# Optimization experiments

Hardware: AMD Instinct MI355X
Metric: run time of the kernel (lower is better)

## Reference

```python
import jax, jax.numpy as jnp
import numpy as np

B, N, M, DIN, HID, L, NC, NH = 8, 1024, 8, 1024, 256, 2, 7, 4
DH = HID // NH
ALPHA = 0.1          # LeakyReLU slope in RGATLayer
NEG = -9e15          # masked-softmax fill value from the source


def setup_inputs() -> dict:
    key = jax.random.key(0)
    ks = jax.random.split(key, 40)
    f32 = jnp.float32
    rn = lambda k, s, sc: jax.random.normal(k, s, f32) * sc
    w = HID ** -0.5
    inp = {
        'x': rn(ks[0], (B, N, DIN), 1.0),
        'adj': jax.random.randint(ks[1], (B, N, N), 0, 2, jnp.int32),
        's_mask': jax.random.randint(ks[2], (B, N, N), 0, 2, jnp.int32),
        's_feature': rn(ks[3], (B, M, DIN), 1.0),
        's_adj': jax.random.uniform(ks[4], (B, M, N), f32),
        'speaker_id': jax.random.randint(ks[5], (B, N), 0, M, jnp.int32),
        'fc1_w': rn(ks[6], (DIN, HID), DIN ** -0.5), 'fc1_b': jnp.zeros((HID,), f32),
        'fc2_w': rn(ks[7], (DIN, HID), DIN ** -0.5), 'fc2_b': jnp.zeros((HID,), f32),
        'gat_W': rn(ks[8], (L, HID, HID), w),
        'gat_a': rn(ks[9], (L, 3 * HID), (3 * HID) ** -0.5),
        'rel_emb': rn(ks[10], (L, 2, HID), 0.1),
        'gru_wz': rn(ks[11], (L, HID, HID), 0.1), 'gru_uz': rn(ks[12], (L, HID, HID), 0.1),
        'gru_wr': rn(ks[13], (L, HID, HID), 0.1), 'gru_ur': rn(ks[14], (L, HID, HID), 0.1),
        'gru_w': rn(ks[15], (L, HID, HID), 0.1), 'gru_u': rn(ks[16], (L, HID, HID), 0.1),
        'mha_wv': rn(ks[17], (L, HID, HID), w), 'mha_bv': jnp.zeros((L, HID), f32),
        'mha_wk': rn(ks[18], (L, HID, HID), w), 'mha_bk': jnp.zeros((L, HID), f32),
        'mha_wq': rn(ks[19], (L, HID, HID), w), 'mha_bq': jnp.zeros((L, HID), f32),
        'mha_wo': rn(ks[20], (L, HID, HID), w), 'mha_bo': jnp.zeros((L, HID), f32),
        'ln_g': jnp.ones((L, HID), f32), 'ln_b': jnp.zeros((L, HID), f32),
        'out_w': rn(ks[21], (HID, NC), w), 'out_b': jnp.zeros((NC,), f32),
    }
    return inp


def _layer_norm(x, g, b):
    mu = jnp.mean(x, -1, keepdims=True)
    var = jnp.mean((x - mu) ** 2, -1, keepdims=True)
    return (x - mu) * jax.lax.rsqrt(var + 1e-5) * g + b


def reference(x, adj, s_mask, s_feature, s_adj, speaker_id,
              fc1_w, fc1_b, fc2_w, fc2_b,
              gat_W, gat_a, rel_emb,
              gru_wz, gru_uz, gru_wr, gru_ur, gru_w, gru_u,
              mha_wv, mha_bv, mha_wk, mha_bk, mha_wq, mha_bq, mha_wo, mha_bo,
              ln_g, ln_b, out_w, out_b):
    # eval mode: dropout is identity. init_way == 'global', att_agg == True.
    H = jax.nn.relu(x @ fc1_w + fc1_b)           # [B,N,HID]
    P = jax.nn.relu(s_feature @ fc2_w + fc2_b)   # [B,M,HID]
    adj_mask = adj > 0
    for l in range(L):
        P_l_1 = jnp.einsum('bmn,bmd->bnd', s_adj, P)  # s_adj^T @ P -> [B,N,HID]
        # ---- RGAT layer (decomposed: never materializes [B,N,N,3*HID]) ----
        h = H @ gat_W[l]                               # [B,N,HID]
        a1, a2, a3 = jnp.split(gat_a[l], 3)
        rel_sc = rel_emb[l] @ a3                       # (2,) per-relation score
        e = jax.nn.leaky_relu((h @ a1)[:, :, None] + (h @ a2)[:, None, :]
                              + jnp.take(rel_sc, s_mask), ALPHA)  # [B,N,N]
        att = jax.nn.softmax(jnp.where(adj_mask, e, jnp.float32(NEG)), axis=2)
        Agg = jax.nn.elu(att @ h)                      # [B,N,HID]
        # ---- Multi-head attention aggregation (replicates source's reshape) ----
        V = (H @ mha_wv[l] + mha_bv[l]).reshape(B * NH, -1, DH)
        Km = (P_l_1 @ mha_wk[l] + mha_bk[l]).reshape(B * NH, -1, DH)
        Qm = (Agg @ mha_wq[l] + mha_bq[l]).reshape(B * NH, -1, DH)
        att2 = jax.nn.softmax(jnp.einsum('bqd,bkd->bqk', Qm, Km) * DH ** -0.5, axis=-1)
        ctx = (att2 @ V).reshape(B, -1, HID)
        H_new = _layer_norm(ctx @ mha_wo[l] + mha_bo[l] + H, ln_g[l], ln_b[l])
        # ---- GRU3d speaker-state update (uses H[l], i.e. pre-update H) ----
        P_agg = jnp.einsum('bmn,bnd->bmd', s_adj, H)   # [B,M,HID]
        z = jax.nn.sigmoid(P @ gru_wz[l] + P_agg @ gru_uz[l])
        r = jax.nn.sigmoid(P @ gru_wr[l] + P_agg @ gru_ur[l])
        h_hat = jnp.tanh(P @ gru_w[l] + r * (P_agg @ gru_u[l]))
        P = (1 - z) * P + z * h_hat
        H = H_new
    # sim_loss
    ps = jnp.einsum('bmd,bkd->bmk', P, P)
    ps = ps * (1.0 - jnp.eye(M, dtype=ps.dtype))
    p_sim = jnp.mean(jnp.mean(jnp.mean(ps, -1), -1), -1)
    logits = H @ out_w + out_b
    return (logits, p_sim)
```

## Files before the change

### kernel.cpp

```cpp
#include <hip/hip_runtime.h>
#include <cmath>

#define B 8
#define N 1024
#define MSP 8
#define DIN 1024
#define HID 256
#define NLAYER 2
#define NCLS 7
#define NHEAD 4
#define DHD 64
#define G (B*NHEAD)
#define SEQ 1024
#define LALPHA 0.1f
#define NEGF (-9e15f)
#define RROWS 8

typedef unsigned short u16;
typedef unsigned int u32;
typedef __attribute__((ext_vector_type(8))) short short8;
typedef __attribute__((ext_vector_type(4))) float f32x4;

__device__ __forceinline__ u16 f2bf(float f) {
  u32 u = __float_as_uint(f);
  u += 0x7FFFu + ((u >> 16) & 1u);
  return (u16)(u >> 16);
}
__device__ __forceinline__ float bf2f(u16 v) {
  return __uint_as_float(((u32)v) << 16);
}
__device__ __forceinline__ void stf(float* p, size_t i, float v) { p[i] = v; }
__device__ __forceinline__ void stf(u16* p, size_t i, float v) { p[i] = f2bf(v); }

__device__ __forceinline__ float wave_reduce_sum(float v) {
  #pragma unroll
  for (int o = 32; o > 0; o >>= 1) v += __shfl_xor(v, o, 64);
  return v;
}
__device__ __forceinline__ float wave_reduce_max(float v) {
  #pragma unroll
  for (int o = 32; o > 0; o >>= 1) v = fmaxf(v, __shfl_xor(v, o, 64));
  return v;
}

__device__ __forceinline__ void tcast_tile(
    const float* src, u16* dst, int ldS, int ldD, int r0, int c0, int t,
    u16* tile )
{
  #pragma unroll
  for (int i = 0; i < 4; ++i) {
    int e = i * 1024 + t * 4;
    int r = e >> 6, c = e & 63;
    float4 v = *(const float4*)&src[(size_t)(r0 + r) * ldS + c0 + c];
    u16* d = &tile[r * 72 + c];
    d[0] = f2bf(v.x); d[1] = f2bf(v.y); d[2] = f2bf(v.z); d[3] = f2bf(v.w);
  }
  __syncthreads();
  #pragma unroll
  for (int i = 0; i < 2; ++i) {
    int e = i * 2048 + t * 8;
    int r2 = e >> 6, c2 = e & 63;
    u16 v[8];
    #pragma unroll
    for (int j = 0; j < 8; ++j) v[j] = tile[(c2 + j) * 72 + r2];
    *(uint4*)&dst[(size_t)(c0 + r2) * ldD + r0 + c2] = *(const uint4*)v;
  }
}

__global__ __launch_bounds__(256) void wprep256(
    const float* g, const float* wv, const float* wk, const float* wq,
    const float* wo, const float* wz, const float* wr, const float* w,
    const float* uz, const float* ur, const float* u, u16* WT)
{
  __shared__ u16 tile[64 * 72];
  int z = blockIdx.z, idx = z >> 1, l = z & 1;
  const float* src;
  switch (idx) {
    case 0: src = g; break;  case 1: src = wv; break; case 2: src = wk; break;
    case 3: src = wq; break; case 4: src = wo; break; case 5: src = wz; break;
    case 6: src = wr; break; case 7: src = w; break;  case 8: src = uz; break;
    case 9: src = ur; break; default: src = u; break;
  }
  src += (size_t)l * 65536;
  u16* dst = WT + (size_t)z * 65536;
  tcast_tile(src, dst, 256, 256, blockIdx.x * 64, blockIdx.y * 64, threadIdx.x, tile);
}

__global__ __launch_bounds__(256) void wprepfc(
    const float* w1, const float* w2, u16* WTfc)
{
  __shared__ u16 tile[64 * 72];
  int z = blockIdx.z;
  const float* src = z ? w2 : w1;
  u16* dst = WTfc + (size_t)z * 262144;
  tcast_tile(src, dst, 256, 1024, blockIdx.x * 64, blockIdx.y * 64, threadIdx.x, tile);
}

__global__ __launch_bounds__(256) void utransp_kernel(
    const u16* __restrict__ src, u16* __restrict__ dst, int ldS, int ldD)
{
  __shared__ u16 tile[64 * 72];
  int r0 = blockIdx.x * 64, c0 = blockIdx.y * 64;
  int t = threadIdx.x;
  #pragma unroll
  for (int i = 0; i < 2; ++i) {
    int e = i * 256 + t;
    int sr = e >> 3, d8 = (e & 7) * 8;
    *(uint4*)&tile[sr * 72 + d8] = *(const uint4*)&src[(size_t)(r0 + sr) * ldS + c0 + d8];
  }
  __syncthreads();
  #pragma unroll
  for (int i = 0; i < 2; ++i) {
    int e = i * 256 + t;
    int dr = e >> 3, s8 = (e & 7) * 8;
    u16 v[8];
    #pragma unroll
    for (int j = 0; j < 8; ++j) v[j] = tile[(s8 + j) * 72 + dr];
    *(uint4*)&dst[(size_t)(c0 + dr) * ldD + r0 + s8] = *(const uint4*)v;
  }
}

__global__ __launch_bounds__(256) void outprep(const float* ow, u16* WTout) {
  int t = threadIdx.x;
  for (int e = t; e < NCLS * 256; e += 256) {
    int n = e >> 8, k = e & 255;
    WTout[e] = f2bf(ow[k * NCLS + n]);
  }
}

__device__ __forceinline__ void stage_a(const float* p, u16* d) {
  #pragma unroll
  for (int q = 0; q < 4; ++q) {
    float4 v = *(const float4*)(p + q * 4);
    d[q * 4 + 0] = f2bf(v.x); d[q * 4 + 1] = f2bf(v.y);
    d[q * 4 + 2] = f2bf(v.z); d[q * 4 + 3] = f2bf(v.w);
  }
}
__device__ __forceinline__ void stage_a(const u16* p, u16* d) {
  *(uint4*)d = *(const uint4*)p;
  *(uint4*)(d + 8) = *(const uint4*)(p + 8);
}

template <typename TA, typename TC>
__global__ __launch_bounds__(256) void gemm_t(
    const TA* __restrict__ A, const TA* __restrict__ A2, int zsplit,
    const u16* __restrict__ Wt, const u16* __restrict__ Wt2,
    const float* __restrict__ bias, const float* __restrict__ bias2,
    TC* __restrict__ C,
    int K, int ldA, int ldW, int Nc, int act,
    size_t sA, size_t sW, size_t sC)
{
  __shared__ u16 As[64 * 72];
  __shared__ u16 Ws[64 * 72];
  int z = blockIdx.z;
  const TA* Ab; const u16* Wb; const float* bs;
  if (z < zsplit) {
    Ab = A + (size_t)z * sA; Wb = Wt + (size_t)z * sW; bs = bias;
  } else {
    int z2 = z - zsplit;
    Ab = A2 + (size_t)z2 * sA; Wb = Wt2 + (size_t)z2 * sW; bs = bias2;
  }
  TC* Cb = C + (size_t)z * sC;
  int bm = blockIdx.x * 64, bn = blockIdx.y * 64;
  int t = threadIdx.x;
  int w = t >> 6, lane = t & 63, quad = lane >> 4, l15 = lane & 15;
  int wy = w >> 1, wx = w & 1;
  int sr = t >> 2, kg = (t & 3) * 16;
  bool wok = (bn + sr) < Nc;
  f32x4 acc[2][2];
  #pragma unroll
  for (int i = 0; i < 2; ++i)
    #pragma unroll
    for (int j = 0; j < 2; ++j) acc[i][j] = (f32x4){0.f, 0.f, 0.f, 0.f};

  for (int k0 = 0; k0 < K; k0 += 64) {
    u16 av[16];
    stage_a(Ab + (size_t)(bm + sr) * ldA + k0 + kg, av);
    *(uint4*)&As[sr * 72 + kg] = *(const uint4*)av;
    *(uint4*)&As[sr * 72 + kg + 8] = *(const uint4*)(av + 8);
    if (wok) {
      *(uint4*)&Ws[sr * 72 + kg] = *(const uint4*)(Wb + (size_t)(bn + sr) * ldW + k0 + kg);
      *(uint4*)&Ws[sr * 72 + kg + 8] = *(const uint4*)(Wb + (size_t)(bn + sr) * ldW + k0 + kg + 8);
    } else {
      uint4 zz = {0, 0, 0, 0};
      *(uint4*)&Ws[sr * 72 + kg] = zz;
      *(uint4*)&Ws[sr * 72 + kg + 8] = zz;
    }
    __syncthreads();
    #pragma unroll
    for (int kh = 0; kh < 64; kh += 32) {
      short8 a0 = *(const short8*)&As[(wy * 32 + l15) * 72 + kh + quad * 8];
      short8 a1 = *(const short8*)&As[(wy * 32 + 16 + l15) * 72 + kh + quad * 8];
      short8 b0 = *(const short8*)&Ws[(wx * 32 + l15) * 72 + kh + quad * 8];
      short8 b1 = *(const short8*)&Ws[(wx * 32 + 16 + l15) * 72 + kh + quad * 8];
      acc[0][0] = __builtin_amdgcn_mfma_f32_16x16x32_bf16(a0, b0, acc[0][0], 0, 0, 0);
      acc[0][1] = __builtin_amdgcn_mfma_f32_16x16x32_bf16(a0, b1, acc[0][1], 0, 0, 0);
      acc[1][0] = __builtin_amdgcn_mfma_f32_16x16x32_bf16(a1, b0, acc[1][0], 0, 0, 0);
      acc[1][1] = __builtin_amdgcn_mfma_f32_16x16x32_bf16(a1, b1, acc[1][1], 0, 0, 0);
    }
    __syncthreads();
  }
  #pragma unroll
  for (int sa = 0; sa < 2; ++sa) {
    #pragma unroll
    for (int sb = 0; sb < 2; ++sb) {
      int col = bn + wx * 32 + sb * 16 + l15;
      if (col < Nc) {
        float bv = bs ? bs[col] : 0.f;
        #pragma unroll
        for (int r = 0; r < 4; ++r) {
          int row = bm + wy * 32 + sa * 16 + quad * 4 + r;
          float v = acc[sa][sb][r] + bv;
          if (act == 1) v = fmaxf(v, 0.f);
          else if (act == 2) v = (v > 0.f) ? v : (__expf(v) - 1.f);
          stf(Cb, (size_t)row * Nc + col, v);
        }
      }
    }
  }
}

__global__ __launch_bounds__(256) void fc2_reduce(
    const float* __restrict__ scr, const float* __restrict__ bias,
    float* __restrict__ out)
{
  int i = blockIdx.x * 256 + threadIdx.x;
  float v = scr[i] + scr[16384 + i] + scr[32768 + i] + scr[49152 + i]
          + bias[threadIdx.x];
  out[i] = fmaxf(v, 0.f);
}

__global__ __launch_bounds__(256) void gru_combine(
    const float* __restrict__ zP, const float* __restrict__ zU,
    const float* __restrict__ P, float* __restrict__ Pn)
{
  int i = blockIdx.x * 256 + threadIdx.x;
  float z = 1.f / (1.f + __expf(-(zP[i] + zU[i])));
  float r = 1.f / (1.f + __expf(-(zP[16384 + i] + zU[16384 + i])));
  float hh = tanhf(zP[32768 + i] + r * zU[32768 + i]);
  Pn[i] = (1.f - z) * P[i] + z * hh;
}

__global__ __launch_bounds__(256) void pl1_kernel(
    const float* __restrict__ s_adj, const float* __restrict__ P,
    float* __restrict__ out)
{
  int bn = blockIdx.x;
  int b = bn >> 10, n = bn & 1023, t = threadIdx.x;
  float acc = 0.f;
  #pragma unroll
  for (int m = 0; m < MSP; ++m) {
    float sa = s_adj[(size_t)(b * MSP + m) * N + n];
    acc += sa * P[(size_t)(b * MSP + m) * HID + t];
  }
  out[(size_t)bn * HID + t] = acc;
}

__global__ __launch_bounds__(256) void relsc_kernel(
    const float* __restrict__ rel_emb_l, const float* __restrict__ a3,
    float* __restrict__ rsc)
{
  __shared__ float scratch[4];
  int r = blockIdx.x, t = threadIdx.x;
  float v = rel_emb_l[r * HID + t] * a3[t];
  int wave = t >> 6, lane = t & 63;
  v = wave_reduce_sum(v);
  if (lane == 0) scratch[wave] = v;
  __syncthreads();
  if (t == 0) rsc[r] = scratch[0] + scratch[1] + scratch[2] + scratch[3];
}

__global__ __launch_bounds__(256) void f1f2_kernel(
    const u16* __restrict__ h, const float* __restrict__ a12,
    float* __restrict__ f1, float* __restrict__ f2)
{
  __shared__ float s1[4], s2[4];
  int row = blockIdx.x, t = threadIdx.x;
  float hv = bf2f(h[(size_t)row * HID + t]);
  float v1 = hv * a12[t];
  float v2 = hv * a12[HID + t];
  int wave = t >> 6, lane = t & 63;
  v1 = wave_reduce_sum(v1);
  v2 = wave_reduce_sum(v2);
  if (lane == 0) { s1[wave] = v1; s2[wave] = v2; }
  __syncthreads();
  if (t == 0) f1[row] = s1[0] + s1[1] + s1[2] + s1[3];
  if (t == 1) f2[row] = s2[0] + s2[1] + s2[2] + s2[3];
}

__global__ __launch_bounds__(256) void rgat_scores_kernel(
    const int* __restrict__ adj, const int* __restrict__ smask,
    const float* __restrict__ f1, const float* __restrict__ f2,
    const float* __restrict__ rsc, u16* __restrict__ Pw)
{
  __shared__ float red[4][RROWS];
  int blk = blockIdx.x;
  int b = blk / (N / RROWS);
  int i0 = (blk % (N / RROWS)) * RROWS;
  int t = threadIdx.x;
  int wave = t >> 6, lane = t & 63;
  float r0 = rsc[0], r1 = rsc[1];
  int j0 = t * 4;
  float4 f2v = *(const float4*)&f2[b * N + j0];
  float ev[RROWS][4];
  #pragma unroll
  for (int r = 0; r < RROWS; ++r) {
    size_t base = ((size_t)(b * N + i0 + r)) * N + j0;
    int4 a4 = *(const int4*)&adj[base];
    int4 s4 = *(const int4*)&smask[base];
    float f1v = f1[b * N + i0 + r];
    float e;
    e = f1v + f2v.x + (s4.x ? r1 : r0); e = (e > 0.f) ? e : LALPHA * e;
    ev[r][0] = (a4.x > 0) ? e : NEGF;
    e = f1v + f2v.y + (s4.y ? r1 : r0); e = (e > 0.f) ? e : LALPHA * e;
    ev[r][1] = (a4.y > 0) ? e : NEGF;
    e = f1v + f2v.z + (s4.z ? r1 : r0); e = (e > 0.f) ? e : LALPHA * e;
    ev[r][2] = (a4.z > 0) ? e : NEGF;
    e = f1v + f2v.w + (s4.w ? r1 : r0); e = (e > 0.f) ? e : LALPHA * e;
    ev[r][3] = (a4.w > 0) ? e : NEGF;
  }
  #pragma unroll
  for (int r = 0; r < RROWS; ++r) {
    float m = fmaxf(fmaxf(ev[r][0], ev[r][1]), fmaxf(ev[r][2], ev[r][3]));
    m = wave_reduce_max(m);
    if (lane == 0) red[wave][r] = m;
  }
  __syncthreads();
  float mx[RROWS];
  #pragma unroll
  for (int r = 0; r < RROWS; ++r)
    mx[r] = fmaxf(fmaxf(red[0][r], red[1][r]), fmaxf(red[2][r], red[3][r]));
  __syncthreads();
  #pragma unroll
  for (int r = 0; r < RROWS; ++r) {
    float s = 0.f;
    #pragma unroll
    for (int c = 0; c < 4; ++c) { ev[r][c] = __expf(ev[r][c] - mx[r]); s += ev[r][c]; }
    s = wave_reduce_sum(s);
    if (lane == 0) red[wave][r] = s;
  }
  __syncthreads();
  #pragma unroll
  for (int r = 0; r < RROWS; ++r) {
    float inv = 1.f / (red[0][r] + red[1][r] + red[2][r] + red[3][r]);
    u16 o[4];
    #pragma unroll
    for (int c = 0; c < 4; ++c) o[c] = f2bf(ev[r][c] * inv);
    *(uint2*)&Pw[((size_t)(b * N + i0 + r)) * N + j0] = *(const uint2*)o;
  }
}

__global__ __launch_bounds__(256) void vtransp_kernel(
    const u16* __restrict__ Vb, u16* __restrict__ Vt)
{
  __shared__ u16 tile[64 * 72];
  int g = blockIdx.x >> 4;
  int s0 = (blockIdx.x & 15) * 64;
  int t = threadIdx.x;
  #pragma unroll
  for (int i = 0; i < 2; ++i) {
    int e = i * 256 + t;
    int sr = e >> 3, d8 = (e & 7) * 8;
    *(uint4*)&tile[sr * 72 + d8] =
        *(const uint4*)&Vb[((size_t)(g * SEQ) + s0 + sr) * DHD + d8];
  }
  __syncthreads();
  #pragma unroll
  for (int i = 0; i < 2; ++i) {
    int e = i * 256 + t;
    int dr = e >> 3, s8 = (e & 7) * 8;
    u16 v[8];
    #pragma unroll
    for (int j = 0; j < 8; ++j) v[j] = tile[(s8 + j) * 72 + dr];
    *(uint4*)&Vt[((size_t)(g * DHD) + dr) * SEQ + s0 + s8] = *(const uint4*)v;
  }
}

__global__ __launch_bounds__(256) void mha_mfma_kernel(
    const u16* __restrict__ Qb, const u16* __restrict__ Kb,
    const u16* __restrict__ Vt, float* __restrict__ ctx)
{
  __shared__ u16 Ks[64 * 72];
  __shared__ u16 Vs[64 * 72];
  __shared__ u16 Ps[4][16 * 72];
  int g = blockIdx.x >> 4;
  int q0 = (blockIdx.x & 15) * 64;
  int t = threadIdx.x;
  int w = t >> 6, lane = t & 63, quad = lane >> 4, l15 = lane & 15;
  const u16* Qrow = Qb + ((size_t)(g * SEQ) + q0 + w * 16 + l15) * DHD;
  short8 qa0 = *(const short8*)(Qrow + quad * 8);
  short8 qa1 = *(const short8*)(Qrow + 32 + quad * 8);
  const u16* Kg = Kb + (size_t)g * SEQ * DHD;
  const u16* Vg = Vt + (size_t)g * DHD * SEQ;
  f32x4 O[4];
  #pragma unroll
  for (int nt = 0; nt < 4; ++nt) O[nt] = (f32x4){0.f, 0.f, 0.f, 0.f};
  float mprev[4] = {-1e30f, -1e30f, -1e30f, -1e30f};
  float lsum[4] = {0.f, 0.f, 0.f, 0.f};

  for (int kc = 0; kc < SEQ; kc += 64) {
    #pragma unroll
    for (int i = 0; i < 2; ++i) {
      int e = i * 256 + t;
      int row = e >> 3, c8 = (e & 7) * 8;
      *(uint4*)&Ks[row * 72 + c8] = *(const uint4*)&Kg[(size_t)(kc + row) * DHD + c8];
      *(uint4*)&Vs[row * 72 + c8] = *(const uint4*)&Vg[(size_t)row * SEQ + kc + c8];
    }
    __syncthreads();
    f32x4 s[4];
    #pragma unroll
    for (int st = 0; st < 4; ++st) {
      short8 b0 = *(const short8*)&Ks[(st * 16 + l15) * 72 + quad * 8];
      short8 b1 = *(const short8*)&Ks[(st * 16 + l15) * 72 + 32 + quad * 8];
      f32x4 c = (f32x4){0.f, 0.f, 0.f, 0.f};
      c = __builtin_amdgcn_mfma_f32_16x16x32_bf16(qa0, b0, c, 0, 0, 0);
      c = __builtin_amdgcn_mfma_f32_16x16x32_bf16(qa1, b1, c, 0, 0, 0);
      s[st] = c * 0.125f;
    }
    float cm[4];
    #pragma unroll
    for (int r = 0; r < 4; ++r)
      cm[r] = fmaxf(fmaxf(s[0][r], s[1][r]), fmaxf(s[2][r], s[3][r]));
    #pragma unroll
    for (int off = 1; off < 16; off <<= 1) {
      #pragma unroll
      for (int r = 0; r < 4; ++r) cm[r] = fmaxf(cm[r], __shfl_xor(cm[r], off, 64));
    }
    float mnew[4], alpha[4], rs[4];
    #pragma unroll
    for (int r = 0; r < 4; ++r) {
      mnew[r] = fmaxf(mprev[r], cm[r]);
      alpha[r] = __expf(mprev[r] - mnew[r]);
      mprev[r] = mnew[r];
      rs[r] = 0.f;
    }
    #pragma unroll
    for (int st = 0; st < 4; ++st) {
      #pragma unroll
      for (int r = 0; r < 4; ++r) {
        float p = __expf(s[st][r] - mnew[r]);
        rs[r] += p;
        Ps[w][(quad * 4 + r) * 72 + st * 16 + l15] = f2bf(p);
      }
    }
    #pragma unroll
    for (int off = 1; off < 16; off <<= 1) {
      #pragma unroll
      for (int r = 0; r < 4; ++r) rs[r] += __shfl_xor(rs[r], off, 64);
    }
    #pragma unroll
    for (int r = 0; r < 4; ++r) lsum[r] = lsum[r] * alpha[r] + rs[r];
    #pragma unroll
    for (int nt = 0; nt < 4; ++nt)
      #pragma unroll
      for (int r = 0; r < 4; ++r) O[nt][r] *= alpha[r];
    #pragma unroll
    for (int kh = 0; kh < 2; ++kh) {
      short8 pa = *(const short8*)&Ps[w][l15 * 72 + kh * 32 + quad * 8];
      #pragma unroll
      for (int nt = 0; nt < 4; ++nt) {
        short8 vb = *(const short8*)&Vs[(nt * 16 + l15) * 72 + kh * 32 + quad * 8];
        O[nt] = __builtin_amdgcn_mfma_f32_16x16x32_bf16(pa, vb, O[nt], 0, 0, 0);
      }
    }
    __syncthreads();
  }
  #pragma unroll
  for (int nt = 0; nt < 4; ++nt) {
    #pragma unroll
    for (int r = 0; r < 4; ++r) {
      size_t row = (size_t)(g * SEQ) + q0 + w * 16 + quad * 4 + r;
      ctx[row * DHD + nt * 16 + l15] = O[nt][r] / lsum[r];
    }
  }
}

__global__ __launch_bounds__(256) void ln_kernel(
    const float* __restrict__ tmp, const float* __restrict__ Hres,
    const float* __restrict__ gg, const float* __restrict__ bb,
    float* __restrict__ out)
{
  __shared__ float s1[4], s2[4];
  int row = blockIdx.x, t = threadIdx.x;
  float x = tmp[(size_t)row * HID + t] + Hres[(size_t)row * HID + t];
  float v1 = wave_reduce_sum(x);
  float v2 = wave_reduce_sum(x * x);
  int wave = t >> 6, lane = t & 63;
  if (lane == 0) { s1[wave] = v1; s2[wave] = v2; }
  __syncthreads();
  float mu = (s1[0] + s1[1] + s1[2] + s1[3]) * (1.f / HID);
  float var = (s2[0] + s2[1] + s2[2] + s2[3]) * (1.f / HID) - mu * mu;
  var = fmaxf(var, 0.f);
  float y = (x - mu) * rsqrtf(var + 1e-5f) * gg[t] + bb[t];
  out[(size_t)row * HID + t] = y;
}

__global__ __launch_bounds__(256) void pagg_part(
    const float* __restrict__ s_adj, const float* __restrict__ H,
    float* __restrict__ scr)
{
  int row = blockIdx.x;
  int sl = blockIdx.y;
  int b = row >> 3, t = threadIdx.x;
  const float* Hb = H + ((size_t)(b * N) + sl * 128) * HID + t;
  const float* sa = s_adj + (size_t)row * N + sl * 128;
  float acc = 0.f;
  #pragma unroll 4
  for (int n = 0; n < 128; ++n)
    acc += sa[n] * Hb[(size_t)n * HID];
  scr[((size_t)sl * (B * MSP) + row) * HID + t] = acc;
}
__global__ __launch_bounds__(256) void pagg_reduce(
    const float* __restrict__ scr, float* __restrict__ Pagg)
{
  int row = blockIdx.x, t = threadIdx.x;
  float s = 0.f;
  #pragma unroll
  for (int k = 0; k < 8; ++k) s += scr[((size_t)k * (B * MSP) + row) * HID + t];
  Pagg[(size_t)row * HID + t] = s;
}

__global__ __launch_bounds__(256) void psim_kernel(
    const float* __restrict__ P, float* __restrict__ out)
{
  __shared__ float scratch[4];
  int t = threadIdx.x;
  float total = 0.f;
  for (int idx = t; idx < B * MSP * MSP; idx += 256) {
    int b = idx >> 6, m = (idx >> 3) & 7, k = idx & 7;
    if (m != k) {
      const float* pm = P + (size_t)(b * MSP + m) * HID;
      const float* pk = P + (size_t)(b * MSP + k) * HID;
      float d = 0.f;
      for (int dd = 0; dd < HID; ++dd) d += pm[dd] * pk[dd];
      total += d;
    }
  }
  int wave = t >> 6, lane = t & 63;
  total = wave_reduce_sum(total);
  if (lane == 0) scratch[wave] = total;
  __syncthreads();
  if (t == 0)
    out[0] = (scratch[0] + scratch[1] + scratch[2] + scratch[3]) *
             (1.f / (B * MSP * MSP));
}

extern "C" void kernel_launch(void* const* d_in, const int* in_sizes, int n_in,
                              void* d_out, int out_size, void* d_ws, size_t ws_size,
                              hipStream_t stream) {
  const float* x      = (const float*)d_in[0];
  const int*   adj    = (const int*)d_in[1];
  const int*   smask  = (const int*)d_in[2];
  const float* s_feat = (const float*)d_in[3];
  const float* s_adj  = (const float*)d_in[4];
  const float* fc1_w  = (const float*)d_in[6];
  const float* fc1_b  = (const float*)d_in[7];
  const float* fc2_w  = (const float*)d_in[8];
  const float* fc2_b  = (const float*)d_in[9];
  const float* gat_W  = (const float*)d_in[10];
  const float* gat_a  = (const float*)d_in[11];
  const float* rel_emb= (const float*)d_in[12];
  const float* gru_wz = (const float*)d_in[13];
  const float* gru_uz = (const float*)d_in[14];
  const float* gru_wr = (const float*)d_in[15];
  const float* gru_ur = (const float*)d_in[16];
  const float* gru_w  = (const float*)d_in[17];
  const float* gru_u  = (const float*)d_in[18];
  const float* mha_wv = (const float*)d_in[19];
  const float* mha_bv = (const float*)d_in[20];
  const float* mha_wk = (const float*)d_in[21];
  const float* mha_bk = (const float*)d_in[22];
  const float* mha_wq = (const float*)d_in[23];
  const float* mha_bq = (const float*)d_in[24];
  const float* mha_wo = (const float*)d_in[25];
  const float* mha_bo = (const float*)d_in[26];
  const float* ln_g   = (const float*)d_in[27];
  const float* ln_b   = (const float*)d_in[28];
  const float* out_w  = (const float*)d_in[29];
  const float* out_b  = (const float*)d_in[30];

  float* ws = (float*)d_ws;
  const size_t BIG = (size_t)B * N * HID;
  float* H0  = ws + 0 * BIG;
  float* H1  = ws + 1 * BIG;
  u16* hb16 = (u16*)(ws + 2 * BIG);
  u16* Vb16 = hb16 + BIG;
  float* Pl1 = ws + 3 * BIG;
  float* Agg = ws + 4 * BIG;
  u16* Pw   = (u16*)(ws + 5 * BIG);
  u16* Qb16 = (u16*)(ws + 5 * BIG);
  u16* Kb16 = Qb16 + BIG;
  u16* Vt16 = (u16*)(ws + 6 * BIG);
  u16* ht   = (u16*)(ws + 7 * BIG);
  u16* WT   = ht + 2097152;
  u16* WTfc = WT + 22 * 65536;
  u16* WTout= WTfc + 2 * 262144;
  float* scrFc = Agg;
  float* zP = Pl1;
  float* zU = Pl1 + 3 * 16384;
  float* paggScr = Pl1 + 6 * 16384;
  float* smw = ws + 8 * BIG;
  float* P0   = smw;
  float* P1   = smw + 16384;
  float* Pagg = smw + 32768;
  float* f1   = smw + 49152;
  float* f2   = smw + 57344;
  float* rsc  = smw + 65536;

  dim3 blk(256);
  const size_t W64K = 65536;

  wprep256<<<dim3(4, 4, 22), blk, 0, stream>>>(
      gat_W, mha_wv, mha_wk, mha_wq, mha_wo,
      gru_wz, gru_wr, gru_w, gru_uz, gru_ur, gru_u, WT);
  wprepfc<<<dim3(16, 4, 2), blk, 0, stream>>>(fc1_w, fc2_w, WTfc);
  outprep<<<1, blk, 0, stream>>>(out_w, WTout);

  gemm_t<float, float><<<dim3(128, 4, 1), blk, 0, stream>>>(
      x, x, 99, WTfc, WTfc, fc1_b, fc1_b, H0, DIN, DIN, DIN, HID, 1, 0, 0, 0);
  gemm_t<float, float><<<dim3(1, 4, 4), blk, 0, stream>>>(
      s_feat, s_feat, 99, WTfc + 262144, WTfc, nullptr, nullptr, scrFc,
      256, DIN, DIN, HID, 0, 256, 256, 16384);
  fc2_reduce<<<64, blk, 0, stream>>>(scrFc, fc2_b, P0);

  float* Hc = H0; float* Hn = H1; float* Pc = P0; float* Pn = P1;
  for (int l = 0; l < NLAYER; ++l) {
    pl1_kernel<<<B * N, blk, 0, stream>>>(s_adj, Pc, Pl1);
    gemm_t<float, u16><<<dim3(128, 4, 2), blk, 0, stream>>>(
        Hc, Hc, 1, WT + (size_t)(0 + l) * W64K, WT + (size_t)(2 + l) * W64K,
        nullptr, mha_bv + l * HID, hb16, HID, HID, HID, HID, 0, 0, 0, BIG);
    utransp_kernel<<<dim3(128, 4), blk, 0, stream>>>(hb16, ht, HID, B * N);
    relsc_kernel<<<2, blk, 0, stream>>>(rel_emb + (size_t)l * 2 * HID,
                                        gat_a + (size_t)l * 3 * HID + 2 * HID, rsc);
    f1f2_kernel<<<B * N, blk, 0, stream>>>(hb16, gat_a + (size_t)l * 3 * HID, f1, f2);
    rgat_scores_kernel<<<B * (N / RROWS), blk, 0, stream>>>(adj, smask, f1, f2, rsc, Pw);
    gemm_t<u16, float><<<dim3(16, 4, 8), blk, 0, stream>>>(
        Pw, Pw, 99, ht, ht, nullptr, nullptr, Agg, N, N, B * N, HID, 2,
        (size_t)N * N, (size_t)N, (size_t)N * HID);
    gemm_t<float, u16><<<dim3(128, 4, 2), blk, 0, stream>>>(
        Agg, Pl1, 1, WT + (size_t)(6 + l) * W64K, WT + (size_t)(4 + l) * W64K,
        mha_bq + l * HID, mha_bk + l * HID, Qb16, HID, HID, HID, HID, 0, 0, 0, BIG);
    vtransp_kernel<<<G * (SEQ / 64), blk, 0, stream>>>(Vb16, Vt16);
    mha_mfma_kernel<<<G * (SEQ / 64), blk, 0, stream>>>(Qb16, Kb16, Vt16, Agg);
    gemm_t<float, float><<<dim3(128, 4, 1), blk, 0, stream>>>(
        Agg, Agg, 99, WT + (size_t)(8 + l) * W64K, WT, mha_bo + l * HID, nullptr,
        Pl1, HID, HID, HID, HID, 0, 0, 0, 0);
    ln_kernel<<<B * N, blk, 0, stream>>>(Pl1, Hc, ln_g + l * HID, ln_b + l * HID, Hn);
    pagg_part<<<dim3(B * MSP, 8), blk, 0, stream>>>(s_adj, Hc, paggScr);
    pagg_reduce<<<B * MSP, blk, 0, stream>>>(paggScr, Pagg);
    gemm_t<float, float><<<dim3(1, 4, 6), blk, 0, stream>>>(
        Pc, Pagg, 3, WT + (size_t)(10 + l) * W64K, WT + (size_t)(16 + l) * W64K,
        nullptr, nullptr, zP, HID, HID, HID, HID, 0, 0, 2 * W64K, 16384);
    gru_combine<<<64, blk, 0, stream>>>(zP, zU, Pc, Pn);
    float* th = Hc; Hc = Hn; Hn = th;
    float* tp = Pc; Pc = Pn; Pn = tp;
  }
  gemm_t<float, float><<<dim3(128, 1, 1), blk, 0, stream>>>(
      Hc, Hc, 99, WTout, WTout, out_b, out_b, (float*)d_out,
      HID, HID, HID, NCLS, 0, 0, 0, 0);
  psim_kernel<<<1, blk, 0, stream>>>(Pc, (float*)d_out + (size_t)B * N * NCLS);
}
```

Baseline: 549.3 us.

## Split MHA attention over key halves and merge partials in a combine kernel

The flash-style MHA kernel now launches twice as many blocks, each covering half of the key sequence. Each block writes its unnormalized output together with the running max and sum, and a new combine kernel merges the two halves with a log-sum-exp rescale. The intent is to raise occupancy across the GPU's compute units, since the original 512-block grid may underfill the device. The cost is extra global traffic for the partials and one more launch. The relation-score kernel is also hoisted out of the layer loop and computed once for both layers.

```diff
diff --git a/kernel.cpp b/kernel.cpp
--- a/kernel.cpp
+++ b/kernel.cpp
@@ -12,6 +12,7 @@
 #define DHD 64
 #define G (B*NHEAD)
 #define SEQ 1024
+#define GSEQ (G*SEQ)
 #define LALPHA 0.1f
 #define NEGF (-9e15f)
 #define RROWS 8
@@ -257,17 +258,19 @@
 }
 
 __global__ __launch_bounds__(256) void relsc_kernel(
-    const float* __restrict__ rel_emb_l, const float* __restrict__ a3,
+    const float* __restrict__ rel_emb, const float* __restrict__ gat_a,
     float* __restrict__ rsc)
 {
   __shared__ float scratch[4];
-  int r = blockIdx.x, t = threadIdx.x;
-  float v = rel_emb_l[r * HID + t] * a3[t];
+  int z = blockIdx.x, l = z >> 1, r = z & 1, t = threadIdx.x;
+  const float* re = rel_emb + ((size_t)l * 2 + r) * HID;
+  const float* a3 = gat_a + (size_t)l * 3 * HID + 2 * HID;
+  float v = re[t] * a3[t];
   int wave = t >> 6, lane = t & 63;
   v = wave_reduce_sum(v);
   if (lane == 0) scratch[wave] = v;
   __syncthreads();
-  if (t == 0) rsc[r] = scratch[0] + scratch[1] + scratch[2] + scratch[3];
+  if (t == 0) rsc[z] = scratch[0] + scratch[1] + scratch[2] + scratch[3];
 }
 
 __global__ __launch_bounds__(256) void f1f2_kernel(
@@ -378,13 +381,19 @@
 
 __global__ __launch_bounds__(256) void mha_mfma_kernel(
     const u16* __restrict__ Qb, const u16* __restrict__ Kb,
-    const u16* __restrict__ Vt, float* __restrict__ ctx)
+    const u16* __restrict__ Vt,
+    float* __restrict__ Opart0, float* __restrict__ Opart1,
+    float* __restrict__ mscr, float* __restrict__ lscr)
 {
   __shared__ u16 Ks[64 * 72];
   __shared__ u16 Vs[64 * 72];
   __shared__ u16 Ps[4][16 * 72];
-  int g = blockIdx.x >> 4;
-  int q0 = (blockIdx.x & 15) * 64;
+  int blk = blockIdx.x;
+  int ks = blk & 1;
+  int gq = blk >> 1;
+  int g = gq >> 4;
+  int q0 = (gq & 15) * 64;
+  int kbase = ks * (SEQ / 2);
   int t = threadIdx.x;
   int w = t >> 6, lane = t & 63, quad = lane >> 4, l15 = lane & 15;
   const u16* Qrow = Qb + ((size_t)(g * SEQ) + q0 + w * 16 + l15) * DHD;
@@ -398,7 +407,7 @@
   float mprev[4] = {-1e30f, -1e30f, -1e30f, -1e30f};
   float lsum[4] = {0.f, 0.f, 0.f, 0.f};
 
-  for (int kc = 0; kc < SEQ; kc += 64) {
+  for (int kc = kbase; kc < kbase + SEQ / 2; kc += 64) {
     #pragma unroll
     for (int i = 0; i < 2; ++i) {
       int e = i * 256 + t;
@@ -465,14 +474,37 @@
     }
     __syncthreads();
   }
+  float* Op = ks ? Opart1 : Opart0;
   #pragma unroll
   for (int nt = 0; nt < 4; ++nt) {
     #pragma unroll
     for (int r = 0; r < 4; ++r) {
       size_t row = (size_t)(g * SEQ) + q0 + w * 16 + quad * 4 + r;
-      ctx[row * DHD + nt * 16 + l15] = O[nt][r] / lsum[r];
-    }
-  }
+      Op[row * DHD + nt * 16 + l15] = O[nt][r];
+    }
+  }
+  if (l15 == 0) {
+    #pragma unroll
+    for (int r = 0; r < 4; ++r) {
+      size_t row = (size_t)(g * SEQ) + q0 + w * 16 + quad * 4 + r;
+      mscr[(size_t)ks * GSEQ + row] = mprev[r];
+      lscr[(size_t)ks * GSEQ + row] = lsum[r];
+    }
+  }
+}
+
+__global__ __launch_bounds__(256) void mha_combine(
+    const float* __restrict__ Opart0, const float* __restrict__ Opart1,
+    const float* __restrict__ mscr, const float* __restrict__ lscr,
+    float* __restrict__ ctx)
+{
+  int i = blockIdx.x * 256 + threadIdx.x;
+  int row = i >> 6;
+  float m1 = mscr[row], m2 = mscr[GSEQ + row];
+  float l1 = lscr[row], l2 = lscr[GSEQ + row];
+  float m = fmaxf(m1, m2);
+  float a1 = __expf(m1 - m), a2 = __expf(m2 - m);
+  ctx[i] = (Opart0[i] * a1 + Opart1[i] * a2) / (l1 * a1 + l2 * a2);
 }
 
 __global__ __launch_bounds__(256) void ln_kernel(
@@ -605,7 +637,9 @@
   float* Pagg = smw + 32768;
   float* f1   = smw + 49152;
   float* f2   = smw + 57344;
-  float* rsc  = smw + 65536;
+  float* rsc4 = smw + 65536;
+  float* mscr = smw + 131072;
+  float* lscr = smw + 196608;
 
   dim3 blk(256);
   const size_t W64K = 65536;
@@ -615,6 +649,7 @@
       gru_wz, gru_wr, gru_w, gru_uz, gru_ur, gru_u, WT);
   wprepfc<<<dim3(16, 4, 2), blk, 0, stream>>>(fc1_w, fc2_w, WTfc);
   outprep<<<1, blk, 0, stream>>>(out_w, WTout);
+  relsc_kernel<<<4, blk, 0, stream>>>(rel_emb, gat_a, rsc4);
 
   gemm_t<float, float><<<dim3(128, 4, 1), blk, 0, stream>>>(
       x, x, 99, WTfc, WTfc, fc1_b, fc1_b, H0, DIN, DIN, DIN, HID, 1, 0, 0, 0);
@@ -630,10 +665,9 @@
         Hc, Hc, 1, WT + (size_t)(0 + l) * W64K, WT + (size_t)(2 + l) * W64K,
         nullptr, mha_bv + l * HID, hb16, HID, HID, HID, HID, 0, 0, 0, BIG);
     utransp_kernel<<<dim3(128, 4), blk, 0, stream>>>(hb16, ht, HID, B * N);
-    relsc_kernel<<<2, blk, 0, stream>>>(rel_emb + (size_t)l * 2 * HID,
-                                        gat_a + (size_t)l * 3 * HID + 2 * HID, rsc);
     f1f2_kernel<<<B * N, blk, 0, stream>>>(hb16, gat_a + (size_t)l * 3 * HID, f1, f2);
-    rgat_scores_kernel<<<B * (N / RROWS), blk, 0, stream>>>(adj, smask, f1, f2, rsc, Pw);
+    rgat_scores_kernel<<<B * (N / RROWS), blk, 0, stream>>>(adj, smask, f1, f2,
+                                                           rsc4 + l * 2, Pw);
     gemm_t<u16, float><<<dim3(16, 4, 8), blk, 0, stream>>>(
         Pw, Pw, 99, ht, ht, nullptr, nullptr, Agg, N, N, B * N, HID, 2,
         (size_t)N * N, (size_t)N, (size_t)N * HID);
@@ -641,7 +675,9 @@
         Agg, Pl1, 1, WT + (size_t)(6 + l) * W64K, WT + (size_t)(4 + l) * W64K,
         mha_bq + l * HID, mha_bk + l * HID, Qb16, HID, HID, HID, HID, 0, 0, 0, BIG);
     vtransp_kernel<<<G * (SEQ / 64), blk, 0, stream>>>(Vb16, Vt16);
-    mha_mfma_kernel<<<G * (SEQ / 64), blk, 0, stream>>>(Qb16, Kb16, Vt16, Agg);
+    mha_mfma_kernel<<<G * (SEQ / 64) * 2, blk, 0, stream>>>(
+        Qb16, Kb16, Vt16, Hn, Pl1, mscr, lscr);
+    mha_combine<<<GSEQ * DHD / 256, blk, 0, stream>>>(Hn, Pl1, mscr, lscr, Agg);
     gemm_t<float, float><<<dim3(128, 4, 1), blk, 0, stream>>>(
         Agg, Agg, 99, WT + (size_t)(8 + l) * W64K, WT, mha_bo + l * HID, nullptr,
         Pl1, HID, HID, HID, HID, 0, 0, 0, 0);
```

Measured after the change: 551.2 us. No clear change (+0.3%).

## Fuse RGAT masked softmax and aggregation GEMM into flash-style kernel

Applied to the files above, without the earlier changes.

Replaces the separate RGAT score/softmax kernel and the P@h GEMM with one online-softmax kernel. Each block streams adjacency and mask chunks, keeps running max and sum, and accumulates P·h with bf16 MFMA, applying ELU at the end. This avoids writing and re-reading the B×N×N bf16 attention matrix. It also hoists the relation-score kernel out of the layer loop into one launch. In exchange there are only 256 blocks, each rescaling its accumulators per chunk and reloading the h tile for every 32-row block, so parallelism and h reuse are lower.

```diff
diff --git a/kernel.cpp b/kernel.cpp
--- a/kernel.cpp
+++ b/kernel.cpp
@@ -12,9 +12,9 @@
 #define DHD 64
 #define G (B*NHEAD)
 #define SEQ 1024
+#define GSEQ (G*SEQ)
 #define LALPHA 0.1f
 #define NEGF (-9e15f)
-#define RROWS 8
 
 typedef unsigned short u16;
 typedef unsigned int u32;
@@ -257,17 +257,19 @@
 }
 
 __global__ __launch_bounds__(256) void relsc_kernel(
-    const float* __restrict__ rel_emb_l, const float* __restrict__ a3,
+    const float* __restrict__ rel_emb, const float* __restrict__ gat_a,
     float* __restrict__ rsc)
 {
   __shared__ float scratch[4];
-  int r = blockIdx.x, t = threadIdx.x;
-  float v = rel_emb_l[r * HID + t] * a3[t];
+  int z = blockIdx.x, l = z >> 1, r = z & 1, t = threadIdx.x;
+  const float* re = rel_emb + ((size_t)l * 2 + r) * HID;
+  const float* a3 = gat_a + (size_t)l * 3 * HID + 2 * HID;
+  float v = re[t] * a3[t];
   int wave = t >> 6, lane = t & 63;
   v = wave_reduce_sum(v);
   if (lane == 0) scratch[wave] = v;
   __syncthreads();
-  if (t == 0) rsc[r] = scratch[0] + scratch[1] + scratch[2] + scratch[3];
+  if (t == 0) rsc[z] = scratch[0] + scratch[1] + scratch[2] + scratch[3];
 }
 
 __global__ __launch_bounds__(256) void f1f2_kernel(
@@ -288,65 +290,110 @@
   if (t == 1) f2[row] = s2[0] + s2[1] + s2[2] + s2[3];
 }
 
-__global__ __launch_bounds__(256) void rgat_scores_kernel(
+__global__ __launch_bounds__(256) void flash_rgat_kernel(
     const int* __restrict__ adj, const int* __restrict__ smask,
     const float* __restrict__ f1, const float* __restrict__ f2,
-    const float* __restrict__ rsc, u16* __restrict__ Pw)
-{
-  __shared__ float red[4][RROWS];
+    const float* __restrict__ rsc, const u16* __restrict__ ht,
+    float* __restrict__ Agg)
+{
+  __shared__ u16 hs[256 * 72];
+  __shared__ u16 Ps[32 * 72];
+  __shared__ float al_s[32], l_s[32];
   int blk = blockIdx.x;
-  int b = blk / (N / RROWS);
-  int i0 = (blk % (N / RROWS)) * RROWS;
+  int b = blk >> 5;
+  int i0 = (blk & 31) * 32;
   int t = threadIdx.x;
-  int wave = t >> 6, lane = t & 63;
+  int w = t >> 6, lane = t & 63, quad = lane >> 4, l15 = lane & 15;
+  int rowbase = (w & 1) * 16, colbase = (w >> 1) * 128;
+  int brow = t >> 3;
+  int bk0 = (t & 7) * 8;
   float r0 = rsc[0], r1 = rsc[1];
-  int j0 = t * 4;
-  float4 f2v = *(const float4*)&f2[b * N + j0];
-  float ev[RROWS][4];
-  #pragma unroll
-  for (int r = 0; r < RROWS; ++r) {
-    size_t base = ((size_t)(b * N + i0 + r)) * N + j0;
+  float f1v = f1[b * N + i0 + brow];
+  float mrun = -1e30f, lrun = 0.f;
+  f32x4 O[8];
+  #pragma unroll
+  for (int nt = 0; nt < 8; ++nt) O[nt] = (f32x4){0.f, 0.f, 0.f, 0.f};
+
+  for (int kc = 0; kc < N; kc += 64) {
+    __syncthreads();
+    const u16* htb = ht + (size_t)b * N + kc;
+    #pragma unroll
+    for (int i = 0; i < 8; ++i) {
+      int e = i * 256 + t;
+      int d = e >> 3, k8 = (e & 7) * 8;
+      *(uint4*)&hs[d * 72 + k8] = *(const uint4*)&htb[(size_t)d * (B * N) + k8];
+    }
+    float4 f2a = *(const float4*)&f2[b * N + kc + bk0];
+    float4 f2c = *(const float4*)&f2[b * N + kc + bk0 + 4];
+    size_t base = ((size_t)(b * N + i0 + brow)) * N + kc + bk0;
     int4 a4 = *(const int4*)&adj[base];
+    int4 a5 = *(const int4*)&adj[base + 4];
     int4 s4 = *(const int4*)&smask[base];
-    float f1v = f1[b * N + i0 + r];
-    float e;
-    e = f1v + f2v.x + (s4.x ? r1 : r0); e = (e > 0.f) ? e : LALPHA * e;
-    ev[r][0] = (a4.x > 0) ? e : NEGF;
-    e = f1v + f2v.y + (s4.y ? r1 : r0); e = (e > 0.f) ? e : LALPHA * e;
-    ev[r][1] = (a4.y > 0) ? e : NEGF;
-    e = f1v + f2v.z + (s4.z ? r1 : r0); e = (e > 0.f) ? e : LALPHA * e;
-    ev[r][2] = (a4.z > 0) ? e : NEGF;
-    e = f1v + f2v.w + (s4.w ? r1 : r0); e = (e > 0.f) ? e : LALPHA * e;
-    ev[r][3] = (a4.w > 0) ? e : NEGF;
-  }
-  #pragma unroll
-  for (int r = 0; r < RROWS; ++r) {
-    float m = fmaxf(fmaxf(ev[r][0], ev[r][1]), fmaxf(ev[r][2], ev[r][3]));
-    m = wave_reduce_max(m);
-    if (lane == 0) red[wave][r] = m;
-  }
+    int4 s5 = *(const int4*)&smask[base + 4];
+    float e8[8];
+    {
+      float e;
+      e = f1v + f2a.x + (s4.x ? r1 : r0); e = (e > 0.f) ? e : LALPHA * e; e8[0] = (a4.x > 0) ? e : NEGF;
+      e = f1v + f2a.y + (s4.y ? r1 : r0); e = (e > 0.f) ? e : LALPHA * e; e8[1] = (a4.y > 0) ? e : NEGF;
+      e = f1v + f2a.z + (s4.z ? r1 : r0); e = (e > 0.f) ? e : LALPHA * e; e8[2] = (a4.z > 0) ? e : NEGF;
+      e = f1v + f2a.w + (s4.w ? r1 : r0); e = (e > 0.f) ? e : LALPHA * e; e8[3] = (a4.w > 0) ? e : NEGF;
+      e = f1v + f2c.x + (s5.x ? r1 : r0); e = (e > 0.f) ? e : LALPHA * e; e8[4] = (a5.x > 0) ? e : NEGF;
+      e = f1v + f2c.y + (s5.y ? r1 : r0); e = (e > 0.f) ? e : LALPHA * e; e8[5] = (a5.y > 0) ? e : NEGF;
+      e = f1v + f2c.z + (s5.z ? r1 : r0); e = (e > 0.f) ? e : LALPHA * e; e8[6] = (a5.z > 0) ? e : NEGF;
+      e = f1v + f2c.w + (s5.w ? r1 : r0); e = (e > 0.f) ? e : LALPHA * e; e8[7] = (a5.w > 0) ? e : NEGF;
+    }
+    float cm = e8[0];
+    #pragma unroll
+    for (int j = 1; j < 8; ++j) cm = fmaxf(cm, e8[j]);
+    #pragma unroll
+    for (int off = 1; off < 8; off <<= 1) cm = fmaxf(cm, __shfl_xor(cm, off, 64));
+    float mnew = fmaxf(mrun, cm);
+    float alpha = __expf(mrun - mnew);
+    mrun = mnew;
+    float rs = 0.f;
+    u16 o8[8];
+    #pragma unroll
+    for (int j = 0; j < 8; ++j) {
+      float p = __expf(e8[j] - mnew);
+      rs += p;
+      o8[j] = f2bf(p);
+    }
+    *(uint4*)&Ps[brow * 72 + bk0] = *(const uint4*)o8;
+    #pragma unroll
+    for (int off = 1; off < 8; off <<= 1) rs += __shfl_xor(rs, off, 64);
+    lrun = lrun * alpha + rs;
+    if ((t & 7) == 0) al_s[brow] = alpha;
+    __syncthreads();
+    float ar[4];
+    #pragma unroll
+    for (int r = 0; r < 4; ++r) ar[r] = al_s[rowbase + quad * 4 + r];
+    #pragma unroll
+    for (int nt = 0; nt < 8; ++nt)
+      #pragma unroll
+      for (int r = 0; r < 4; ++r) O[nt][r] *= ar[r];
+    #pragma unroll
+    for (int kh = 0; kh < 2; ++kh) {
+      short8 pa = *(const short8*)&Ps[(rowbase + l15) * 72 + kh * 32 + quad * 8];
+      #pragma unroll
+      for (int nt = 0; nt < 8; ++nt) {
+        short8 vb = *(const short8*)&hs[(colbase + nt * 16 + l15) * 72 + kh * 32 + quad * 8];
+        O[nt] = __builtin_amdgcn_mfma_f32_16x16x32_bf16(pa, vb, O[nt], 0, 0, 0);
+      }
+    }
+  }
+  if ((t & 7) == 0) l_s[brow] = lrun;
   __syncthreads();
-  float mx[RROWS];
-  #pragma unroll
-  for (int r = 0; r < RROWS; ++r)
-    mx[r] = fmaxf(fmaxf(red[0][r], red[1][r]), fmaxf(red[2][r], red[3][r]));
-  __syncthreads();
-  #pragma unroll
-  for (int r = 0; r < RROWS; ++r) {
-    float s = 0.f;
-    #pragma unroll
-    for (int c = 0; c < 4; ++c) { ev[r][c] = __expf(ev[r][c] - mx[r]); s += ev[r][c]; }
-    s = wave_reduce_sum(s);
-    if (lane == 0) red[wave][r] = s;
-  }
-  __syncthreads();
-  #pragma unroll
-  for (int r = 0; r < RROWS; ++r) {
-    float inv = 1.f / (red[0][r] + red[1][r] + red[2][r] + red[3][r]);
-    u16 o[4];
-    #pragma unroll
-    for (int c = 0; c < 4; ++c) o[c] = f2bf(ev[r][c] * inv);
-    *(uint2*)&Pw[((size_t)(b * N + i0 + r)) * N + j0] = *(const uint2*)o;
+  float li[4];
+  #pragma unroll
+  for (int r = 0; r < 4; ++r) li[r] = 1.f / l_s[rowbase + quad * 4 + r];
+  #pragma unroll
+  for (int nt = 0; nt < 8; ++nt) {
+    #pragma unroll
+    for (int r = 0; r < 4; ++r) {
+      float v = O[nt][r] * li[r];
+      v = (v > 0.f) ? v : (__expf(v) - 1.f);
+      Agg[((size_t)(b * N + i0 + rowbase + quad * 4 + r)) * HID + colbase + nt * 16 + l15] = v;
+    }
   }
 }
 
@@ -587,7 +634,6 @@
   u16* Vb16 = hb16 + BIG;
   float* Pl1 = ws + 3 * BIG;
   float* Agg = ws + 4 * BIG;
-  u16* Pw   = (u16*)(ws + 5 * BIG);
   u16* Qb16 = (u16*)(ws + 5 * BIG);
   u16* Kb16 = Qb16 + BIG;
   u16* Vt16 = (u16*)(ws + 6 * BIG);
@@ -605,7 +651,7 @@
   float* Pagg = smw + 32768;
   float* f1   = smw + 49152;
   float* f2   = smw + 57344;
-  float* rsc  = smw + 65536;
+  float* rsc4 = smw + 65536;
 
   dim3 blk(256);
   const size_t W64K = 65536;
@@ -615,6 +661,7 @@
       gru_wz, gru_wr, gru_w, gru_uz, gru_ur, gru_u, WT);
   wprepfc<<<dim3(16, 4, 2), blk, 0, stream>>>(fc1_w, fc2_w, WTfc);
   outprep<<<1, blk, 0, stream>>>(out_w, WTout);
+  relsc_kernel<<<4, blk, 0, stream>>>(rel_emb, gat_a, rsc4);
 
   gemm_t<float, float><<<dim3(128, 4, 1), blk, 0, stream>>>(
       x, x, 99, WTfc, WTfc, fc1_b, fc1_b, H0, DIN, DIN, DIN, HID, 1, 0, 0, 0);
@@ -630,13 +677,9 @@
         Hc, Hc, 1, WT + (size_t)(0 + l) * W64K, WT + (size_t)(2 + l) * W64K,
         nullptr, mha_bv + l * HID, hb16, HID, HID, HID, HID, 0, 0, 0, BIG);
     utransp_kernel<<<dim3(128, 4), blk, 0, stream>>>(hb16, ht, HID, B * N);
-    relsc_kernel<<<2, blk, 0, stream>>>(rel_emb + (size_t)l * 2 * HID,
-                                        gat_a + (size_t)l * 3 * HID + 2 * HID, rsc);
     f1f2_kernel<<<B * N, blk, 0, stream>>>(hb16, gat_a + (size_t)l * 3 * HID, f1, f2);
-    rgat_scores_kernel<<<B * (N / RROWS), blk, 0, stream>>>(adj, smask, f1, f2, rsc, Pw);
-    gemm_t<u16, float><<<dim3(16, 4, 8), blk, 0, stream>>>(
-        Pw, Pw, 99, ht, ht, nullptr, nullptr, Agg, N, N, B * N, HID, 2,
-        (size_t)N * N, (size_t)N, (size_t)N * HID);
+    flash_rgat_kernel<<<B * (N / 32), blk, 0, stream>>>(
+        adj, smask, f1, f2, rsc4 + l * 2, ht, Agg);
     gemm_t<float, u16><<<dim3(128, 4, 2), blk, 0, stream>>>(
         Agg, Pl1, 1, WT + (size_t)(6 + l) * W64K, WT + (size_t)(4 + l) * W64K,
         mha_bq + l * HID, mha_bk + l * HID, Qb16, HID, HID, HID, HID, 0, 0, 0, BIG);
```

Result: slower. 586.9 us (+6.8%).
